# Optimization experiments

Measured on AMD Instinct MI355X. Metric: run time of the kernel, lower is better.

Reference implementation:

```python
import jax, jax.numpy as jnp
import numpy as np

DIM = 128
NUM_LAYERS = 2
FF_MULT = 4
RADIUS = 0.2
K = 8
B, N, L = 8, 2048, 4096
NEG = -1e30


def setup_inputs() -> dict:
    key = jax.random.key(0)
    ks = jax.random.split(key, 12)
    C = DIM
    s = 1.0 / np.sqrt(C)
    w = lambda k, shape, sc: jax.random.normal(k, shape, dtype=jnp.float32) * sc
    inp = {
        "q_xyz": jax.random.uniform(ks[0], (B, N, 3), dtype=jnp.float32),
        "q_feat": jax.random.normal(ks[1], (B, N, C), dtype=jnp.float32),
        "kv_xyz": jax.random.uniform(ks[2], (B, L, 3), dtype=jnp.float32),
        "kv_feat": jax.random.normal(ks[3], (B, L, C), dtype=jnp.float32),
        "kv_pad": jnp.zeros((B, L), dtype=bool),
        # PointTransformerConv params (stacked over layers)
        "W_lin": w(ks[4], (NUM_LAYERS, C, C), s),   # value projection (with bias)
        "b_lin": jnp.zeros((NUM_LAYERS, C), jnp.float32),
        "W_src": w(ks[5], (NUM_LAYERS, C, C), s),   # lin_src, no bias
        "W_dst": w(ks[6], (NUM_LAYERS, C, C), s),   # lin_dst, no bias
        "W_attn": w(ks[7], (NUM_LAYERS, C, C), s),  # attn_nn = Linear+ReLU
        "b_attn": jnp.zeros((NUM_LAYERS, C), jnp.float32),
        "ln1_g": jnp.ones((NUM_LAYERS, C), jnp.float32),
        "ln1_b": jnp.zeros((NUM_LAYERS, C), jnp.float32),
        "W_ff1": w(ks[8], (NUM_LAYERS, C, FF_MULT * C), s),
        "b_ff1": jnp.zeros((NUM_LAYERS, FF_MULT * C), jnp.float32),
        "W_ff2": w(ks[9], (NUM_LAYERS, FF_MULT * C, C), 1.0 / np.sqrt(FF_MULT * C)),
        "b_ff2": jnp.zeros((NUM_LAYERS, C), jnp.float32),
        "ln2_g": jnp.ones((NUM_LAYERS, C), jnp.float32),
        "ln2_b": jnp.zeros((NUM_LAYERS, C), jnp.float32),
    }
    return inp


def _layernorm(x, g, b):
    mu = x.mean(-1, keepdims=True)
    var = ((x - mu) ** 2).mean(-1, keepdims=True)
    return (x - mu) * jax.lax.rsqrt(var + 1e-5) * g + b


def _gather(feats, idx):
    # feats: [B, L, C], idx: [B, N, K] -> [B, N, K, C]
    b, n, k = idx.shape
    g = jnp.take_along_axis(feats, idx.reshape(b, n * k)[:, :, None], axis=1)
    return g.reshape(b, n, k, feats.shape[-1])


def _forward(q_xyz, q_feat, kv_xyz, kv_feat, kv_pad,
             W_lin, b_lin, W_src, W_dst, W_attn, b_attn,
             ln1_g, ln1_b, W_ff1, b_ff1, W_ff2, b_ff2, ln2_g, ln2_b):
    # radius neighbor search (per-batch, fixed K neighbors with validity mask)
    d2 = jnp.sum((q_xyz[:, :, None, :] - kv_xyz[:, None, :, :]) ** 2, axis=-1)  # [B,N,L]
    valid_pair = (d2 <= RADIUS * RADIUS) & (~kv_pad)[:, None, :]
    negd = jnp.where(valid_pair, -d2, NEG)
    negv, idx = jax.lax.top_k(negd, K)          # [B,N,K] nearest-in-ball
    evalid = negv > 0.5 * NEG                   # edge validity mask [B,N,K]

    out = q_feat
    for i in range(NUM_LAYERS):
        # PointTransformerConv, pos_nn = ZeroPos => delta = 0
        aj = _gather(kv_feat @ W_src[i], idx)                    # [B,N,K,C]
        vj = _gather(kv_feat @ W_lin[i] + b_lin[i], idx)         # [B,N,K,C]
        ai = out @ W_dst[i]                                      # [B,N,C]
        logits = jax.nn.relu((ai[:, :, None, :] - aj) @ W_attn[i] + b_attn[i])
        logits = jnp.where(evalid[..., None], logits, NEG)
        m = logits.max(axis=2, keepdims=True)
        e = jnp.exp(logits - m) * evalid[..., None]
        attn = e / jnp.maximum(e.sum(axis=2, keepdims=True), 1e-9)  # per-channel softmax over neighbors
        upd = jnp.sum(attn * vj, axis=2)                         # [B,N,C] scatter-add over edges
        out = _layernorm(out + upd, ln1_g[i], ln1_b[i])
        h = jax.nn.gelu(out @ W_ff1[i] + b_ff1[i], approximate=False)
        out = _layernorm(out + h @ W_ff2[i] + b_ff2[i], ln2_g[i], ln2_b[i])
    return out


def reference(q_xyz, q_feat, kv_xyz, kv_feat, kv_pad,
              W_lin, b_lin, W_src, W_dst, W_attn, b_attn,
              ln1_g, ln1_b, W_ff1, b_ff1, W_ff2, b_ff2, ln2_g, ln2_b):
    return _forward(q_xyz, q_feat, kv_xyz, kv_feat, kv_pad,
                    W_lin, b_lin, W_src, W_dst, W_attn, b_attn,
                    ln1_g, ln1_b, W_ff1, b_ff1, W_ff2, b_ff2, ln2_g, ln2_b)
```

## Files before the change

kernel.cpp:

```cpp
#include <hip/hip_runtime.h>
#include <hip/hip_bf16.h>
#include <math.h>

#define DIM 128
#define BB 8
#define NN 2048
#define LL 4096
#define KK 8

typedef __hip_bfloat16 bf16;
typedef unsigned long long ull;
typedef __attribute__((ext_vector_type(8))) short short8;
typedef __attribute__((ext_vector_type(4))) float float4v;

__device__ __forceinline__ float toF(float x){ return x; }
__device__ __forceinline__ float toF(bf16 x){ return __bfloat162float(x); }
__device__ __forceinline__ void st(float* p, float v){ *p = v; }
__device__ __forceinline__ void st(bf16*  p, float v){ *p = __float2bfloat16(v); }
__device__ __forceinline__ unsigned short f2bf(float f){
  union { bf16 b; unsigned short u; } cv; cv.b = __float2bfloat16(f); return cv.u;
}
__device__ __forceinline__ float2 ld2bf(const bf16* p){
  const unsigned u = *(const unsigned*)p;
  return make_float2(__uint_as_float(u << 16), __uint_as_float(u & 0xFFFF0000u));
}
__device__ __forceinline__ void st2bf(bf16* p, float a, float b){
  *(unsigned*)p = (unsigned)f2bf(a) | ((unsigned)f2bf(b) << 16);
}

__device__ __forceinline__ float gelu_exact(float x){
  return 0.5f * x * (1.0f + erff(x * 0.70710678118654752f));
}

__device__ __forceinline__ float waveSum64(float v){
  #pragma unroll
  for (int o = 32; o > 0; o >>= 1) v += __shfl_xor(v, o, 64);
  return v;
}
__device__ __forceinline__ float quadSum16(float v){
  #pragma unroll
  for (int o = 8; o > 0; o >>= 1) v += __shfl_xor(v, o, 64);
  return v;
}

__device__ __forceinline__ void topk_insert_u(ull (&m)[KK], ull key){
  m[KK-1] = key;
  #pragma unroll
  for (int t = KK-1; t > 0; --t){
    if (m[t] < m[t-1]){ ull tmp = m[t]; m[t] = m[t-1]; m[t-1] = tmp; }
  }
}

#define NC3 125
__device__ __forceinline__ void packOne(const float* __restrict__ src,
                                        bf16* __restrict__ dst, int idx, int nshift){
  const int k = idx >> nshift;
  const int n = idx & ((1 << nshift) - 1);
  const int N = 1 << nshift;
  st(&dst[((size_t)(k>>3)*N + n)*8 + (k&7)], src[idx]);
}

__global__ __launch_bounds__(1024) void setup_all(const float* __restrict__ kv_xyz,
                                                  const float* __restrict__ q_xyz,
                                                  float4* __restrict__ bpts,
                                                  int* __restrict__ offs,
                                                  int* __restrict__ qsrt,
                                                  const float* __restrict__ Wlin,
                                                  const float* __restrict__ Wff1,
                                                  const float* __restrict__ Wff2,
                                                  const float* __restrict__ Wsrc,
                                                  const float* __restrict__ Wdst,
                                                  const float* __restrict__ Wattn,
                                                  bf16* __restrict__ WlinP,
                                                  bf16* __restrict__ Wff1P,
                                                  bf16* __restrict__ Wff2P,
                                                  bf16* __restrict__ WsaP,
                                                  bf16* __restrict__ WdaP)
{
  __shared__ int cnt[NC3];
  __shared__ int off[NC3+1];
  __shared__ float row[8][DIM];
  const int bid = blockIdx.x;
  const int tid = threadIdx.x;
  if (bid < 16){
    const int b   = bid & 7;
    const int role= bid >> 3;
    if (tid < NC3) cnt[tid] = 0;
    __syncthreads();
    if (role == 0){
      const float* kvp = kv_xyz + (size_t)b * LL * 3;
      float px[4], py[4], pz[4]; int pc[4];
      #pragma unroll
      for (int i = 0; i < 4; i++){
        const int e = tid + i*1024;
        px[i] = kvp[3*e]; py[i] = kvp[3*e+1]; pz[i] = kvp[3*e+2];
        const int cx = min((int)(px[i]*5.f), 4);
        const int cy = min((int)(py[i]*5.f), 4);
        const int cz = min((int)(pz[i]*5.f), 4);
        pc[i] = (cz*5 + cy)*5 + cx;
        atomicAdd(&cnt[pc[i]], 1);
      }
      __syncthreads();
      if (tid == 0){
        int acc = 0;
        for (int c = 0; c < NC3; c++){ off[c] = acc; acc += cnt[c]; }
        off[NC3] = acc;
      }
      __syncthreads();
      if (tid < NC3) cnt[tid] = 0;
      __syncthreads();
      float4* dst = bpts + (size_t)b * LL;
      #pragma unroll
      for (int i = 0; i < 4; i++){
        const int e = tid + i*1024;
        const int pos = off[pc[i]] + atomicAdd(&cnt[pc[i]], 1);
        dst[pos] = make_float4(px[i], py[i], pz[i], __int_as_float(e));
      }
      if (tid < NC3 + 1) offs[b*126 + tid] = off[tid];
    } else {
      const float* qp = q_xyz + (size_t)b * NN * 3;
      int pc[2];
      #pragma unroll
      for (int i = 0; i < 2; i++){
        const int e = tid + i*1024;
        const float x = qp[3*e], y = qp[3*e+1], z = qp[3*e+2];
        const int cx = min((int)(x*5.f), 4);
        const int cy = min((int)(y*5.f), 4);
        const int cz = min((int)(z*5.f), 4);
        pc[i] = (cz*5 + cy)*5 + cx;
        atomicAdd(&cnt[pc[i]], 1);
      }
      __syncthreads();
      if (tid == 0){
        int acc = 0;
        for (int c = 0; c < NC3; c++){ off[c] = acc; acc += cnt[c]; }
        off[NC3] = acc;
      }
      __syncthreads();
      if (tid < NC3) cnt[tid] = 0;
      __syncthreads();
      int* dst = qsrt + (size_t)b * NN;
      #pragma unroll
      for (int i = 0; i < 2; i++){
        const int e = tid + i*1024;
        const int pos = off[pc[i]] + atomicAdd(&cnt[pc[i]], 1);
        dst[pos] = e;
      }
    }
  } else if (bid < 304){
    int i = (bid - 16)*1024 + tid;
    if (i < 32768){
      const int l = i >> 14, r = i & 16383;
      packOne(Wlin + (size_t)l*16384, WlinP + (size_t)l*16384, r, 7);
    } else if (i < 163840){
      i -= 32768;
      const int l = i >> 16, r = i & 65535;
      packOne(Wff1 + (size_t)l*65536, Wff1P + (size_t)l*65536, r, 9);
    } else {
      i -= 163840;
      const int l = i >> 16, r = i & 65535;
      packOne(Wff2 + (size_t)l*65536, Wff2P + (size_t)l*65536, r, 7);
    }
  } else {
    const int grp = tid >> 7;
    const int c = tid & 127;
    const int tt = (bid - 304)*8 + grp;
    const int r = tt & 127, which = (tt >> 7) & 1, lay = tt >> 8;
    const float* Wx = (which ? Wdst : Wsrc) + (size_t)lay*DIM*DIM;
    const float* Wa = Wattn + (size_t)lay*DIM*DIM;
    row[grp][c] = Wx[r*DIM + c];
    __syncthreads();
    float acc = 0.f;
    for (int j = 0; j < DIM; j++) acc = fmaf(row[grp][j], Wa[j*DIM + c], acc);
    bf16* dst = (which ? WdaP : WsaP) + (size_t)lay*DIM*DIM;
    st(&dst[((size_t)(r>>3)*DIM + c)*8 + (r&7)], acc);
  }
}

#define QBLK 8
#define SPL 32
__global__ __launch_bounds__(256) void knn_query(const float* __restrict__ q_xyz,
                                                 const float4* __restrict__ bpts,
                                                 const int* __restrict__ offs,
                                                 const int* __restrict__ qsrt,
                                                 int* __restrict__ idx)
{
  __shared__ ull cd[QBLK*257];
  const int tid  = threadIdx.x;
  const int s    = tid & 31;
  const int qloc = tid >> 5;
  const int b    = blockIdx.y;
  const int qbase = blockIdx.x * QBLK;
  const int qid = qsrt[b*NN + qbase + qloc];
  const size_t qo = ((size_t)b * NN + qid) * 3;
  const float qx = q_xyz[qo], qy = q_xyz[qo+1], qz = q_xyz[qo+2];
  const ull THRKEY = ((ull)0x3D23D70Bu << 32);
  ull kthr = THRKEY;
  ull m[KK];
  #pragma unroll
  for (int k = 0; k < KK; k++) m[k] = ~0ULL;
  const int qcx = min((int)(qx*5.f), 4);
  const int qcy = min((int)(qy*5.f), 4);
  const int qcz = min((int)(qz*5.f), 4);
  const int* ofb = offs + b*126;
  const float4* bp = bpts + (size_t)b * LL;
  const int cx0 = max(qcx-1, 0), cx1 = min(qcx+1, 4);
  for (int cz = max(qcz-1,0); cz <= min(qcz+1,4); cz++){
    for (int cy = max(qcy-1,0); cy <= min(qcy+1,4); cy++){
      const int rowc = (cz*5 + cy)*5;
      const int pend = ofb[rowc + cx1 + 1];
      int p = ofb[rowc + cx0] + s;
      if (p < pend){
        float4 pt = bp[p];
        while (true){
          const int pn = p + SPL;
          const bool hn = pn < pend;
          float4 nx;
          if (hn) nx = bp[pn];
          const float dx = qx - pt.x, dy = qy - pt.y, dz = qz - pt.z;
          const float d2 = dx*dx + dy*dy + dz*dz;
          const ull key = ((ull)__float_as_uint(d2) << 32) | (unsigned)__float_as_int(pt.w);
          if (key < kthr){
            topk_insert_u(m, key);
            kthr = (m[KK-1] < THRKEY) ? m[KK-1] : THRKEY;
          }
          if (!hn) break;
          pt = nx; p = pn;
        }
      }
    }
  }
  #pragma unroll
  for (int k = 0; k < KK; k++) cd[qloc*257 + k*32 + s] = m[k];
  __syncthreads();
  if (tid < 64){
    const int q = tid >> 3, g = tid & 7;
    ull mm[KK];
    #pragma unroll
    for (int k = 0; k < KK; k++) mm[k] = ~0ULL;
    #pragma unroll
    for (int u = 0; u < 4; u++){
      const int sl = g + 8*u;
      #pragma unroll
      for (int k = 0; k < KK; k++){
        const ull key = cd[q*257 + k*32 + sl];
        if (key < mm[KK-1]) topk_insert_u(mm, key);
      }
    }
    #pragma unroll
    for (int k = 0; k < KK; k++) cd[q*257 + k*32 + g] = mm[k];
    if (tid < QBLK){
      ull f[KK];
      #pragma unroll
      for (int k = 0; k < KK; k++) f[k] = ~0ULL;
      #pragma unroll
      for (int k = 0; k < 8; k++)
        for (int g2 = 0; g2 < 8; g2++){
          const ull key = cd[tid*257 + k*32 + g2];
          if (key < f[KK-1]) topk_insert_u(f, key);
        }
      const int oq = b * NN + qsrt[b*NN + qbase + tid];
      #pragma unroll
      for (int k = 0; k < KK; k++) idx[oq*KK + k] = (int)(unsigned)(f[k] & 0xFFFFFFFFu);
    }
  }
}

__device__ __forceinline__ void stage_A_f32(const float* __restrict__ A, size_t r0,
                                            int kd, int kc, unsigned short* As, int tid){
  #pragma unroll
  for (int i = 0; i < 8; i++){
    const int f = tid + i*256;
    const int row = f >> 5, c4 = (f & 31) * 4;
    const float4 v = *(const float4*)&A[(r0+row)*kd + kc + c4];
    uint2 u;
    u.x = (unsigned)f2bf(v.x) | ((unsigned)f2bf(v.y) << 16);
    u.y = (unsigned)f2bf(v.z) | ((unsigned)f2bf(v.w) << 16);
    *(uint2*)&As[row*136 + c4] = u;
  }
}
__device__ __forceinline__ void stage_A_bf16(const bf16* __restrict__ A, size_t r0,
                                             int kd, int kc, unsigned short* As, int tid){
  #pragma unroll
  for (int i = 0; i < 8; i++){
    const int f = tid + i*256;
    const int row = f >> 5, c4 = (f & 31) * 4;
    *(uint2*)&As[row*136 + c4] = *(const uint2*)&A[(r0+row)*kd + kc + c4];
  }
}

template<typename TA, int NDIM, bool GELU>
__global__ __launch_bounds__(256) void mfma_single(const TA* __restrict__ A,
                                                   const bf16* __restrict__ Wp,
                                                   const float* __restrict__ bias,
                                                   bf16* __restrict__ Y)
{
  __shared__ __align__(16) unsigned short As[64*136];
  const int tid = threadIdx.x;
  const size_t r0 = (size_t)blockIdx.x * 64;
  const int nblk = blockIdx.y * 128;
  if (sizeof(TA) == 4) stage_A_f32((const float*)A, r0, 128, 0, As, tid);
  else                 stage_A_bf16((const bf16*)A, r0, 128, 0, As, tid);
  __syncthreads();
  const int wid = tid >> 6, ln = tid & 63, qd = ln >> 4, cl = ln & 15;
  float4v acc[8];
  #pragma unroll
  for (int t = 0; t < 8; t++) acc[t] = (float4v){0.f,0.f,0.f,0.f};
  #pragma unroll
  for (int ks = 0; ks < 4; ks++){
    const short8 a = *(const short8*)&As[(wid*16 + cl)*136 + (ks*4 + qd)*8];
    const short8* wb = (const short8*)Wp + (size_t)(ks*4 + qd)*NDIM + nblk + cl;
    #pragma unroll
    for (int t = 0; t < 8; t++){
      const short8 b = wb[t*16];
      acc[t] = __builtin_amdgcn_mfma_f32_16x16x32_bf16(a, b, acc[t], 0, 0, 0);
    }
  }
  #pragma unroll
  for (int t = 0; t < 8; t++){
    const int col = nblk + t*16 + cl;
    const float bv = bias ? bias[col] : 0.f;
    #pragma unroll
    for (int r = 0; r < 4; r++){
      const size_t row = r0 + wid*16 + qd*4 + r;
      float v = acc[t][r] + bv;
      if (GELU) v = gelu_exact(v);
      st(&Y[row*NDIM + col], v);
    }
  }
}

__global__ __launch_bounds__(256) void mfma_dual_qa(const float* __restrict__ kvf,
                                                    const float* __restrict__ featIn,
                                                    const bf16* __restrict__ Wp0,
                                                    const bf16* __restrict__ Wp1,
                                                    const bf16* __restrict__ WpQ,
                                                    const float* __restrict__ bias1,
                                                    bf16* __restrict__ Y0,
                                                    bf16* __restrict__ Y1,
                                                    bf16* __restrict__ Yq)
{
  __shared__ __align__(16) unsigned short As[64*136];
  const int tid = threadIdx.x;
  const int wid = tid >> 6, ln = tid & 63, qd = ln >> 4, cl = ln & 15;
  if (blockIdx.x < 512){
    const size_t r0 = (size_t)blockIdx.x * 64;
    stage_A_f32(kvf, r0, 128, 0, As, tid);
    __syncthreads();
    float4v ac0[8], ac1[8];
    #pragma unroll
    for (int t = 0; t < 8; t++){ ac0[t] = (float4v){0.f,0.f,0.f,0.f}; ac1[t] = (float4v){0.f,0.f,0.f,0.f}; }
    #pragma unroll
    for (int ks = 0; ks < 4; ks++){
      const short8 a = *(const short8*)&As[(wid*16 + cl)*136 + (ks*4 + qd)*8];
      const size_t wo = (size_t)(ks*4 + qd)*DIM + cl;
      const short8* wb0 = (const short8*)Wp0 + wo;
      const short8* wb1 = (const short8*)Wp1 + wo;
      #pragma unroll
      for (int t = 0; t < 8; t++){
        const short8 b0 = wb0[t*16];
        ac0[t] = __builtin_amdgcn_mfma_f32_16x16x32_bf16(a, b0, ac0[t], 0, 0, 0);
        const short8 b1 = wb1[t*16];
        ac1[t] = __builtin_amdgcn_mfma_f32_16x16x32_bf16(a, b1, ac1[t], 0, 0, 0);
      }
    }
    #pragma unroll
    for (int t = 0; t < 8; t++){
      const int col = t*16 + cl;
      const float bv = bias1[col];
      #pragma unroll
      for (int r = 0; r < 4; r++){
        const size_t row = r0 + wid*16 + qd*4 + r;
        st(&Y0[row*DIM + col], ac0[t][r]);
        st(&Y1[row*DIM + col], ac1[t][r] + bv);
      }
    }
  } else {
    const size_t r0 = (size_t)(blockIdx.x - 512) * 64;
    stage_A_f32(featIn, r0, 128, 0, As, tid);
    __syncthreads();
    float4v acc[8];
    #pragma unroll
    for (int t = 0; t < 8; t++) acc[t] = (float4v){0.f,0.f,0.f,0.f};
    #pragma unroll
    for (int ks = 0; ks < 4; ks++){
      const short8 a = *(const short8*)&As[(wid*16 + cl)*136 + (ks*4 + qd)*8];
      const short8* wb = (const short8*)WpQ + (size_t)(ks*4 + qd)*DIM + cl;
      #pragma unroll
      for (int t = 0; t < 8; t++){
        const short8 b = wb[t*16];
        acc[t] = __builtin_amdgcn_mfma_f32_16x16x32_bf16(a, b, acc[t], 0, 0, 0);
      }
    }
    #pragma unroll
    for (int t = 0; t < 8; t++){
      const int col = t*16 + cl;
      #pragma unroll
      for (int r = 0; r < 4; r++){
        const size_t row = r0 + wid*16 + qd*4 + r;
        st(&Yq[row*DIM + col], acc[t][r]);
      }
    }
  }
}

__global__ __launch_bounds__(256) void mfma_ff2ln(const bf16* __restrict__ A,
                                                  const bf16* __restrict__ Wp,
                                                  const float* __restrict__ b2,
                                                  const bf16* __restrict__ resid,
                                                  const float* __restrict__ g,
                                                  const float* __restrict__ bb,
                                                  float* __restrict__ Y)
{
  __shared__ __align__(16) unsigned short As[64*136];
  const int tid = threadIdx.x;
  const size_t r0 = (size_t)blockIdx.x * 64;
  const int wid = tid >> 6, ln = tid & 63, qd = ln >> 4, cl = ln & 15;
  float4v acc[8];
  #pragma unroll
  for (int t = 0; t < 8; t++) acc[t] = (float4v){0.f,0.f,0.f,0.f};
  for (int kc = 0; kc < 512; kc += 128){
    __syncthreads();
    stage_A_bf16(A, r0, 512, kc, As, tid);
    __syncthreads();
    const int k8c = kc >> 3;
    #pragma unroll
    for (int ks = 0; ks < 4; ks++){
      const short8 a = *(const short8*)&As[(wid*16 + cl)*136 + (ks*4 + qd)*8];
      const short8* wb = (const short8*)Wp + (size_t)(k8c + ks*4 + qd)*DIM + cl;
      #pragma unroll
      for (int t = 0; t < 8; t++){
        const short8 b = wb[t*16];
        acc[t] = __builtin_amdgcn_mfma_f32_16x16x32_bf16(a, b, acc[t], 0, 0, 0);
      }
    }
  }
  float v[8][4];
  #pragma unroll
  for (int t = 0; t < 8; t++){
    const int col = t*16 + cl;
    const float bv = b2[col];
    #pragma unroll
    for (int r = 0; r < 4; r++){
      const size_t row = r0 + wid*16 + qd*4 + r;
      v[t][r] = acc[t][r] + bv + toF(resid[row*DIM + col]);
    }
  }
  #pragma unroll
  for (int r = 0; r < 4; r++){
    float s = 0.f;
    #pragma unroll
    for (int t = 0; t < 8; t++) s += v[t][r];
    const float mu = quadSum16(s) * (1.f/DIM);
    float q = 0.f;
    #pragma unroll
    for (int t = 0; t < 8; t++){ const float d = v[t][r] - mu; q += d*d; }
    const float inv = rsqrtf(quadSum16(q) * (1.f/DIM) + 1e-5f);
    const size_t row = r0 + wid*16 + qd*4 + r;
    #pragma unroll
    for (int t = 0; t < 8; t++){
      const int col = t*16 + cl;
      Y[row*DIM + col] = (v[t][r] - mu) * inv * g[col] + bb[col];
    }
  }
}

__global__ __launch_bounds__(256) void attn_ln1(const bf16* __restrict__ qA,
                                                const bf16* __restrict__ srcA,
                                                const bf16* __restrict__ linp,
                                                const int* __restrict__ idx,
                                                const int* __restrict__ qsrt,
                                                const float* __restrict__ b_attn,
                                                const float* __restrict__ feat,
                                                const float* __restrict__ g,
                                                const float* __restrict__ bb,
                                                bf16* __restrict__ out1)
{
  const int tid = threadIdx.x;
  const int wv = tid >> 6, ln = tid & 63;
  const int sp = blockIdx.x * 4 + wv;
  const int b = sp >> 11;
  const int q = b * NN + qsrt[b*NN + (sp & 2047)];
  const bf16* sbase = srcA + (size_t)b * LL * DIM;
  const bf16* vbase = linp + (size_t)b * LL * DIM;
  const int c0 = 2*ln;
  const float2 ba = *(const float2*)&b_attn[c0];
  const float2 qa2 = ld2bf(&qA[(size_t)q*DIM + c0]);
  const float qa0 = qa2.x + ba.x, qa1 = qa2.y + ba.y;
  int ids[KK]; float l0[KK], l1[KK];
  float m0 = -1e30f, m1 = -1e30f;
  #pragma unroll
  for (int k = 0; k < KK; k++){
    const int id = idx[q*KK + k]; ids[k] = id;
    if (id >= 0){
      const float2 s2 = ld2bf(&sbase[(size_t)id*DIM + c0]);
      l0[k] = fmaxf(qa0 - s2.x, 0.f); m0 = fmaxf(m0, l0[k]);
      l1[k] = fmaxf(qa1 - s2.y, 0.f); m1 = fmaxf(m1, l1[k]);
    } else { l0[k] = 0.f; l1[k] = 0.f; }
  }
  float sum0 = 0.f, sum1 = 0.f, upd0 = 0.f, upd1 = 0.f;
  #pragma unroll
  for (int k = 0; k < KK; k++) if (ids[k] >= 0){
    const float e0 = expf(l0[k] - m0); l0[k] = e0; sum0 += e0;
    const float e1 = expf(l1[k] - m1); l1[k] = e1; sum1 += e1;
  }
  if (sum0 > 0.f){
    const float i0 = 1.f / sum0, i1 = 1.f / sum1;
    #pragma unroll
    for (int k = 0; k < KK; k++) if (ids[k] >= 0){
      const float2 v2 = ld2bf(&vbase[(size_t)ids[k]*DIM + c0]);
      upd0 = fmaf(l0[k]*i0, v2.x, upd0);
      upd1 = fmaf(l1[k]*i1, v2.y, upd1);
    }
  }
  const float2 f2 = *(const float2*)&feat[(size_t)q*DIM + c0];
  const float x0 = f2.x + upd0;
  const float x1 = f2.y + upd1;
  const float mu = waveSum64(x0 + x1) * (1.f/DIM);
  const float d0 = x0 - mu, d1 = x1 - mu;
  const float var = waveSum64(d0*d0 + d1*d1) * (1.f/DIM);
  const float inv = rsqrtf(var + 1e-5f);
  const float2 gg = *(const float2*)&g[c0];
  const float2 bbv = *(const float2*)&bb[c0];
  st2bf(&out1[(size_t)q*DIM + c0], d0 * inv * gg.x + bbv.x, d1 * inv * gg.y + bbv.y);
}

extern "C" void kernel_launch(void* const* d_in, const int* in_sizes, int n_in,
                              void* d_out, int out_size, void* d_ws, size_t ws_size,
                              hipStream_t stream)
{
  const float* q_xyz  = (const float*)d_in[0];
  const float* q_feat = (const float*)d_in[1];
  const float* kv_xyz = (const float*)d_in[2];
  const float* kv_feat= (const float*)d_in[3];
  const float* W_lin  = (const float*)d_in[5];
  const float* b_lin  = (const float*)d_in[6];
  const float* W_src  = (const float*)d_in[7];
  const float* W_dst  = (const float*)d_in[8];
  const float* W_attn = (const float*)d_in[9];
  const float* b_attn = (const float*)d_in[10];
  const float* ln1_g  = (const float*)d_in[11];
  const float* ln1_b  = (const float*)d_in[12];
  const float* W_ff1  = (const float*)d_in[13];
  const float* b_ff1  = (const float*)d_in[14];
  const float* W_ff2  = (const float*)d_in[15];
  const float* b_ff2  = (const float*)d_in[16];
  const float* ln2_g  = (const float*)d_in[17];
  const float* ln2_b  = (const float*)d_in[18];
  float* out = (float*)d_out;

  const int MQ  = BB * NN;
  const int MKV = BB * LL;

  char* p = (char*)d_ws;
  int*    idxb  = (int*)p;    p += (size_t)MQ * KK * 4;
  float4* bpts  = (float4*)p; p += (size_t)BB * LL * 16;
  int*    boffs = (int*)p;    p += (size_t)BB * 126 * 4;
  int*    qsrt  = (int*)p;    p += (size_t)BB * NN * 4;
  bf16*  WsaP  = (bf16*)p;  p += (size_t)2 * DIM * DIM * 2;
  bf16*  WdaP  = (bf16*)p;  p += (size_t)2 * DIM * DIM * 2;
  bf16*  WlinP = (bf16*)p;  p += (size_t)2 * DIM * DIM * 2;
  bf16*  Wff1P = (bf16*)p;  p += (size_t)2 * DIM * 4*DIM * 2;
  bf16*  Wff2P = (bf16*)p;  p += (size_t)2 * 4*DIM * DIM * 2;
  float* feat  = (float*)p; p += (size_t)MQ * DIM * 4;
  bf16*  out1  = (bf16*)p;  p += (size_t)MQ * DIM * 2;
  bf16*  srcA  = (bf16*)p;  p += (size_t)MKV * DIM * 2;
  bf16*  linp  = (bf16*)p;  p += (size_t)MKV * DIM * 2;
  bf16*  qA    = (bf16*)p;  p += (size_t)MQ * DIM * 2;
  bf16*  hbuf  = srcA;

  setup_all<<<368, 1024, 0, stream>>>(kv_xyz, q_xyz, bpts, boffs, qsrt,
                                      W_lin, W_ff1, W_ff2, W_src, W_dst, W_attn,
                                      WlinP, Wff1P, Wff2P, WsaP, WdaP);
  knn_query<<<dim3(NN/QBLK, BB), 256, 0, stream>>>(q_xyz, bpts, boffs, qsrt, idxb);

  for (int i = 0; i < 2; i++){
    const size_t w128 = (size_t)i * DIM * DIM;
    const size_t w512 = (size_t)i * DIM * 4*DIM;
    const float* featIn = (i == 0) ? q_feat : feat;

    mfma_dual_qa<<<MKV/64 + MQ/64, 256, 0, stream>>>(kv_feat, featIn,
        WsaP + w128, WlinP + w128, WdaP + w128, b_lin + i*DIM, srcA, linp, qA);
    attn_ln1<<<MQ/4, 256, 0, stream>>>(qA, srcA, linp, idxb, qsrt, b_attn + i*DIM,
                                       featIn, ln1_g + i*DIM, ln1_b + i*DIM, out1);
    mfma_single<bf16, 512, true><<<dim3(MQ/64, 4), 256, 0, stream>>>(
        out1, Wff1P + w512, b_ff1 + i*4*DIM, hbuf);
    float* ydst = (i == 1) ? out : feat;
    mfma_ff2ln<<<MQ/64, 256, 0, stream>>>(hbuf, Wff2P + w512, b_ff2 + i*DIM, out1,
                                          ln2_g + i*DIM, ln2_b + i*DIM, ydst);
  }
}
```

Measured before the change: 288.4 us.

## Fuse KNN search with both layers' kv projections in one interleaved launch

Merges the radius KNN query kernel with the kv-side src/lin projection GEMMs for both layers and the layer-0 query projection into a single launch. GEMM and KNN blocks are interleaved so the compute-heavy MFMA work overlaps with the latency-bound neighbour search. Layer 1's kv projections depend only on kv_feat, so they are hoisted out of the layer loop, and layer 1 runs only a small query-side GEMM. This costs extra workspace for separate per-layer src/lin buffers and a dedicated hidden buffer, and removes one launch per layer.

Result: slower. 296.4 us (+2.8%).

```diff
diff --git a/kernel.cpp b/kernel.cpp
--- a/kernel.cpp
+++ b/kernel.cpp
@@ -177,95 +177,6 @@
   }
 }
 
-#define QBLK 8
-#define SPL 32
-__global__ __launch_bounds__(256) void knn_query(const float* __restrict__ q_xyz,
-                                                 const float4* __restrict__ bpts,
-                                                 const int* __restrict__ offs,
-                                                 const int* __restrict__ qsrt,
-                                                 int* __restrict__ idx)
-{
-  __shared__ ull cd[QBLK*257];
-  const int tid  = threadIdx.x;
-  const int s    = tid & 31;
-  const int qloc = tid >> 5;
-  const int b    = blockIdx.y;
-  const int qbase = blockIdx.x * QBLK;
-  const int qid = qsrt[b*NN + qbase + qloc];
-  const size_t qo = ((size_t)b * NN + qid) * 3;
-  const float qx = q_xyz[qo], qy = q_xyz[qo+1], qz = q_xyz[qo+2];
-  const ull THRKEY = ((ull)0x3D23D70Bu << 32);
-  ull kthr = THRKEY;
-  ull m[KK];
-  #pragma unroll
-  for (int k = 0; k < KK; k++) m[k] = ~0ULL;
-  const int qcx = min((int)(qx*5.f), 4);
-  const int qcy = min((int)(qy*5.f), 4);
-  const int qcz = min((int)(qz*5.f), 4);
-  const int* ofb = offs + b*126;
-  const float4* bp = bpts + (size_t)b * LL;
-  const int cx0 = max(qcx-1, 0), cx1 = min(qcx+1, 4);
-  for (int cz = max(qcz-1,0); cz <= min(qcz+1,4); cz++){
-    for (int cy = max(qcy-1,0); cy <= min(qcy+1,4); cy++){
-      const int rowc = (cz*5 + cy)*5;
-      const int pend = ofb[rowc + cx1 + 1];
-      int p = ofb[rowc + cx0] + s;
-      if (p < pend){
-        float4 pt = bp[p];
-        while (true){
-          const int pn = p + SPL;
-          const bool hn = pn < pend;
-          float4 nx;
-          if (hn) nx = bp[pn];
-          const float dx = qx - pt.x, dy = qy - pt.y, dz = qz - pt.z;
-          const float d2 = dx*dx + dy*dy + dz*dz;
-          const ull key = ((ull)__float_as_uint(d2) << 32) | (unsigned)__float_as_int(pt.w);
-          if (key < kthr){
-            topk_insert_u(m, key);
-            kthr = (m[KK-1] < THRKEY) ? m[KK-1] : THRKEY;
-          }
-          if (!hn) break;
-          pt = nx; p = pn;
-        }
-      }
-    }
-  }
-  #pragma unroll
-  for (int k = 0; k < KK; k++) cd[qloc*257 + k*32 + s] = m[k];
-  __syncthreads();
-  if (tid < 64){
-    const int q = tid >> 3, g = tid & 7;
-    ull mm[KK];
-    #pragma unroll
-    for (int k = 0; k < KK; k++) mm[k] = ~0ULL;
-    #pragma unroll
-    for (int u = 0; u < 4; u++){
-      const int sl = g + 8*u;
-      #pragma unroll
-      for (int k = 0; k < KK; k++){
-        const ull key = cd[q*257 + k*32 + sl];
-        if (key < mm[KK-1]) topk_insert_u(mm, key);
-      }
-    }
-    #pragma unroll
-    for (int k = 0; k < KK; k++) cd[q*257 + k*32 + g] = mm[k];
-    if (tid < QBLK){
-      ull f[KK];
-      #pragma unroll
-      for (int k = 0; k < KK; k++) f[k] = ~0ULL;
-      #pragma unroll
-      for (int k = 0; k < 8; k++)
-        for (int g2 = 0; g2 < 8; g2++){
-          const ull key = cd[tid*257 + k*32 + g2];
-          if (key < f[KK-1]) topk_insert_u(f, key);
-        }
-      const int oq = b * NN + qsrt[b*NN + qbase + tid];
-      #pragma unroll
-      for (int k = 0; k < KK; k++) idx[oq*KK + k] = (int)(unsigned)(f[k] & 0xFFFFFFFFu);
-    }
-  }
-}
-
 __device__ __forceinline__ void stage_A_f32(const float* __restrict__ A, size_t r0,
                                             int kd, int kc, unsigned short* As, int tid){
   #pragma unroll
@@ -286,6 +197,182 @@
     const int f = tid + i*256;
     const int row = f >> 5, c4 = (f & 31) * 4;
     *(uint2*)&As[row*136 + c4] = *(const uint2*)&A[(r0+row)*kd + kc + c4];
+  }
+}
+
+#define QBLK 8
+#define SPL 32
+__global__ __launch_bounds__(256) void knn_gemm(const float* __restrict__ q_xyz,
+                                                const float4* __restrict__ bpts,
+                                                const int* __restrict__ offs,
+                                                const int* __restrict__ qsrt,
+                                                int* __restrict__ idx,
+                                                const float* __restrict__ kvf,
+                                                const float* __restrict__ q_feat,
+                                                const bf16* __restrict__ WsaP,
+                                                const bf16* __restrict__ WlinP,
+                                                const bf16* __restrict__ WdaP0,
+                                                const float* __restrict__ b_lin,
+                                                bf16* __restrict__ srcA0,
+                                                bf16* __restrict__ linp0,
+                                                bf16* __restrict__ srcA1,
+                                                bf16* __restrict__ linp1,
+                                                bf16* __restrict__ qA)
+{
+  __shared__ __align__(16) unsigned char smem[17408];
+  const int bid = blockIdx.x;
+  const int tid = threadIdx.x;
+  bool isGemm; int rid;
+  if (bid < 2560){ isGemm = !(bid & 1); rid = bid >> 1; }
+  else { isGemm = false; rid = 1280 + (bid - 2560); }
+
+  if (isGemm){
+    unsigned short* As = (unsigned short*)smem;
+    const int wid = tid >> 6, ln = tid & 63, qd = ln >> 4, cl = ln & 15;
+    if (rid < 1024){
+      const int lay = rid >> 9;
+      const size_t r0 = (size_t)(rid & 511) * 64;
+      const bf16* Wp0 = WsaP  + (size_t)lay * DIM * DIM;
+      const bf16* Wp1 = WlinP + (size_t)lay * DIM * DIM;
+      const float* bias1 = b_lin + lay * DIM;
+      bf16* Y0 = lay ? srcA1 : srcA0;
+      bf16* Y1 = lay ? linp1 : linp0;
+      stage_A_f32(kvf, r0, 128, 0, As, tid);
+      __syncthreads();
+      float4v ac0[8], ac1[8];
+      #pragma unroll
+      for (int t = 0; t < 8; t++){ ac0[t] = (float4v){0.f,0.f,0.f,0.f}; ac1[t] = (float4v){0.f,0.f,0.f,0.f}; }
+      #pragma unroll
+      for (int ks = 0; ks < 4; ks++){
+        const short8 a = *(const short8*)&As[(wid*16 + cl)*136 + (ks*4 + qd)*8];
+        const size_t wo = (size_t)(ks*4 + qd)*DIM + cl;
+        const short8* wb0 = (const short8*)Wp0 + wo;
+        const short8* wb1 = (const short8*)Wp1 + wo;
+        #pragma unroll
+        for (int t = 0; t < 8; t++){
+          const short8 b0 = wb0[t*16];
+          ac0[t] = __builtin_amdgcn_mfma_f32_16x16x32_bf16(a, b0, ac0[t], 0, 0, 0);
+          const short8 b1 = wb1[t*16];
+          ac1[t] = __builtin_amdgcn_mfma_f32_16x16x32_bf16(a, b1, ac1[t], 0, 0, 0);
+        }
+      }
+      #pragma unroll
+      for (int t = 0; t < 8; t++){
+        const int col = t*16 + cl;
+        const float bv = bias1[col];
+        #pragma unroll
+        for (int r = 0; r < 4; r++){
+          const size_t row = r0 + wid*16 + qd*4 + r;
+          st(&Y0[row*DIM + col], ac0[t][r]);
+          st(&Y1[row*DIM + col], ac1[t][r] + bv);
+        }
+      }
+    } else {
+      const size_t r0 = (size_t)(rid - 1024) * 64;
+      stage_A_f32(q_feat, r0, 128, 0, As, tid);
+      __syncthreads();
+      float4v acc[8];
+      #pragma unroll
+      for (int t = 0; t < 8; t++) acc[t] = (float4v){0.f,0.f,0.f,0.f};
+      #pragma unroll
+      for (int ks = 0; ks < 4; ks++){
+        const short8 a = *(const short8*)&As[(wid*16 + cl)*136 + (ks*4 + qd)*8];
+        const short8* wb = (const short8*)WdaP0 + (size_t)(ks*4 + qd)*DIM + cl;
+        #pragma unroll
+        for (int t = 0; t < 8; t++){
+          const short8 b = wb[t*16];
+          acc[t] = __builtin_amdgcn_mfma_f32_16x16x32_bf16(a, b, acc[t], 0, 0, 0);
+        }
+      }
+      #pragma unroll
+      for (int t = 0; t < 8; t++){
+        const int col = t*16 + cl;
+        #pragma unroll
+        for (int r = 0; r < 4; r++){
+          const size_t row = r0 + wid*16 + qd*4 + r;
+          st(&qA[row*DIM + col], acc[t][r]);
+        }
+      }
+    }
+  } else {
+    ull* cd = (ull*)smem;
+    const int s    = tid & 31;
+    const int qloc = tid >> 5;
+    const int b    = rid >> 8;
+    const int qbase = (rid & 255) * QBLK;
+    const int qid = qsrt[b*NN + qbase + qloc];
+    const size_t qo = ((size_t)b * NN + qid) * 3;
+    const float qx = q_xyz[qo], qy = q_xyz[qo+1], qz = q_xyz[qo+2];
+    const ull THRKEY = ((ull)0x3D23D70Bu << 32);
+    ull kthr = THRKEY;
+    ull m[KK];
+    #pragma unroll
+    for (int k = 0; k < KK; k++) m[k] = ~0ULL;
+    const int qcx = min((int)(qx*5.f), 4);
+    const int qcy = min((int)(qy*5.f), 4);
+    const int qcz = min((int)(qz*5.f), 4);
+    const int* ofb = offs + b*126;
+    const float4* bp = bpts + (size_t)b * LL;
+    const int cx0 = max(qcx-1, 0), cx1 = min(qcx+1, 4);
+    for (int cz = max(qcz-1,0); cz <= min(qcz+1,4); cz++){
+      for (int cy = max(qcy-1,0); cy <= min(qcy+1,4); cy++){
+        const int rowc = (cz*5 + cy)*5;
+        const int pend = ofb[rowc + cx1 + 1];
+        int p = ofb[rowc + cx0] + s;
+        if (p < pend){
+          float4 pt = bp[p];
+          while (true){
+            const int pn = p + SPL;
+            const bool hn = pn < pend;
+            float4 nx;
+            if (hn) nx = bp[pn];
+            const float dx = qx - pt.x, dy = qy - pt.y, dz = qz - pt.z;
+            const float d2 = dx*dx + dy*dy + dz*dz;
+            const ull key = ((ull)__float_as_uint(d2) << 32) | (unsigned)__float_as_int(pt.w);
+            if (key < kthr){
+              topk_insert_u(m, key);
+              kthr = (m[KK-1] < THRKEY) ? m[KK-1] : THRKEY;
+            }
+            if (!hn) break;
+            pt = nx; p = pn;
+          }
+        }
+      }
+    }
+    #pragma unroll
+    for (int k = 0; k < KK; k++) cd[qloc*257 + k*32 + s] = m[k];
+    __syncthreads();
+    if (tid < 64){
+      const int q = tid >> 3, g = tid & 7;
+      ull mm[KK];
+      #pragma unroll
+      for (int k = 0; k < KK; k++) mm[k] = ~0ULL;
+      #pragma unroll
+      for (int u = 0; u < 4; u++){
+        const int sl = g + 8*u;
+        #pragma unroll
+        for (int k = 0; k < KK; k++){
+          const ull key = cd[q*257 + k*32 + sl];
+          if (key < mm[KK-1]) topk_insert_u(mm, key);
+        }
+      }
+      #pragma unroll
+      for (int k = 0; k < KK; k++) cd[q*257 + k*32 + g] = mm[k];
+      if (tid < QBLK){
+        ull f[KK];
+        #pragma unroll
+        for (int k = 0; k < KK; k++) f[k] = ~0ULL;
+        #pragma unroll
+        for (int k = 0; k < 8; k++)
+          for (int g2 = 0; g2 < 8; g2++){
+            const ull key = cd[tid*257 + k*32 + g2];
+            if (key < f[KK-1]) topk_insert_u(f, key);
+          }
+        const int oq = b * NN + qsrt[b*NN + qbase + tid];
+        #pragma unroll
+        for (int k = 0; k < KK; k++) idx[oq*KK + k] = (int)(unsigned)(f[k] & 0xFFFFFFFFu);
+      }
+    }
   }
 }
 
@@ -326,80 +413,6 @@
       float v = acc[t][r] + bv;
       if (GELU) v = gelu_exact(v);
       st(&Y[row*NDIM + col], v);
-    }
-  }
-}
-
-__global__ __launch_bounds__(256) void mfma_dual_qa(const float* __restrict__ kvf,
-                                                    const float* __restrict__ featIn,
-                                                    const bf16* __restrict__ Wp0,
-                                                    const bf16* __restrict__ Wp1,
-                                                    const bf16* __restrict__ WpQ,
-                                                    const float* __restrict__ bias1,
-                                                    bf16* __restrict__ Y0,
-                                                    bf16* __restrict__ Y1,
-                                                    bf16* __restrict__ Yq)
-{
-  __shared__ __align__(16) unsigned short As[64*136];
-  const int tid = threadIdx.x;
-  const int wid = tid >> 6, ln = tid & 63, qd = ln >> 4, cl = ln & 15;
-  if (blockIdx.x < 512){
-    const size_t r0 = (size_t)blockIdx.x * 64;
-    stage_A_f32(kvf, r0, 128, 0, As, tid);
-    __syncthreads();
-    float4v ac0[8], ac1[8];
-    #pragma unroll
-    for (int t = 0; t < 8; t++){ ac0[t] = (float4v){0.f,0.f,0.f,0.f}; ac1[t] = (float4v){0.f,0.f,0.f,0.f}; }
-    #pragma unroll
-    for (int ks = 0; ks < 4; ks++){
-      const short8 a = *(const short8*)&As[(wid*16 + cl)*136 + (ks*4 + qd)*8];
-      const size_t wo = (size_t)(ks*4 + qd)*DIM + cl;
-      const short8* wb0 = (const short8*)Wp0 + wo;
-      const short8* wb1 = (const short8*)Wp1 + wo;
-      #pragma unroll
-      for (int t = 0; t < 8; t++){
-        const short8 b0 = wb0[t*16];
-        ac0[t] = __builtin_amdgcn_mfma_f32_16x16x32_bf16(a, b0, ac0[t], 0, 0, 0);
-        const short8 b1 = wb1[t*16];
-        ac1[t] = __builtin_amdgcn_mfma_f32_16x16x32_bf16(a, b1, ac1[t], 0, 0, 0);
-      }
-    }
-    #pragma unroll
-    for (int t = 0; t < 8; t++){
-      const int col = t*16 + cl;
-      const float bv = bias1[col];
-      #pragma unroll
-      for (int r = 0; r < 4; r++){
-        const size_t row = r0 + wid*16 + qd*4 + r;
-        st(&Y0[row*DIM + col], ac0[t][r]);
-        st(&Y1[row*DIM + col], ac1[t][r] + bv);
-      }
-    }
-  } else {
-    const size_t r0 = (size_t)(blockIdx.x - 512) * 64;
-    stage_A_f32(featIn, r0, 128, 0, As, tid);
-    __syncthreads();
-    float4v acc[8];
-    #pragma unroll
-    for (int t = 0; t < 8; t++) acc[t] = (float4v){0.f,0.f,0.f,0.f};
-    #pragma unroll
-    for (int ks = 0; ks < 4; ks++){
-      const short8 a = *(const short8*)&As[(wid*16 + cl)*136 + (ks*4 + qd)*8];
-      const short8* wb = (const short8*)WpQ + (size_t)(ks*4 + qd)*DIM + cl;
-      #pragma unroll
-      for (int t = 0; t < 8; t++){
-        const short8 b = wb[t*16];
-        acc[t] = __builtin_amdgcn_mfma_f32_16x16x32_bf16(a, b, acc[t], 0, 0, 0);
-      }
-    }
-    #pragma unroll
-    for (int t = 0; t < 8; t++){
-      const int col = t*16 + cl;
-      #pragma unroll
-      for (int r = 0; r < 4; r++){
-        const size_t row = r0 + wid*16 + qd*4 + r;
-        st(&Yq[row*DIM + col], acc[t][r]);
-      }
     }
   }
 }
@@ -564,23 +577,30 @@
   bf16*  Wff2P = (bf16*)p;  p += (size_t)2 * 4*DIM * DIM * 2;
   float* feat  = (float*)p; p += (size_t)MQ * DIM * 4;
   bf16*  out1  = (bf16*)p;  p += (size_t)MQ * DIM * 2;
-  bf16*  srcA  = (bf16*)p;  p += (size_t)MKV * DIM * 2;
-  bf16*  linp  = (bf16*)p;  p += (size_t)MKV * DIM * 2;
+  bf16*  srcA0 = (bf16*)p;  p += (size_t)MKV * DIM * 2;
+  bf16*  linp0 = (bf16*)p;  p += (size_t)MKV * DIM * 2;
+  bf16*  srcA1 = (bf16*)p;  p += (size_t)MKV * DIM * 2;
+  bf16*  linp1 = (bf16*)p;  p += (size_t)MKV * DIM * 2;
   bf16*  qA    = (bf16*)p;  p += (size_t)MQ * DIM * 2;
-  bf16*  hbuf  = srcA;
+  bf16*  hbuf  = (bf16*)p;  p += (size_t)MQ * 4*DIM * 2;
 
   setup_all<<<368, 1024, 0, stream>>>(kv_xyz, q_xyz, bpts, boffs, qsrt,
                                       W_lin, W_ff1, W_ff2, W_src, W_dst, W_attn,
                                       WlinP, Wff1P, Wff2P, WsaP, WdaP);
-  knn_query<<<dim3(NN/QBLK, BB), 256, 0, stream>>>(q_xyz, bpts, boffs, qsrt, idxb);
+  knn_gemm<<<3328, 256, 0, stream>>>(q_xyz, bpts, boffs, qsrt, idxb,
+                                     kv_feat, q_feat, WsaP, WlinP, WdaP,
+                                     b_lin, srcA0, linp0, srcA1, linp1, qA);
 
   for (int i = 0; i < 2; i++){
-    const size_t w128 = (size_t)i * DIM * DIM;
     const size_t w512 = (size_t)i * DIM * 4*DIM;
     const float* featIn = (i == 0) ? q_feat : feat;
-
-    mfma_dual_qa<<<MKV/64 + MQ/64, 256, 0, stream>>>(kv_feat, featIn,
-        WsaP + w128, WlinP + w128, WdaP + w128, b_lin + i*DIM, srcA, linp, qA);
+    const bf16* srcA = i ? srcA1 : srcA0;
+    const bf16* linp = i ? linp1 : linp0;
+
+    if (i == 1){
+      mfma_single<float, 128, false><<<MQ/64, 256, 0, stream>>>(
+          feat, WdaP + DIM*DIM, nullptr, qA);
+    }
     attn_ln1<<<MQ/4, 256, 0, stream>>>(qA, srcA, linp, idxb, qsrt, b_attn + i*DIM,
                                        featIn, ln1_g + i*DIM, ln1_b + i*DIM, out1);
     mfma_single<bf16, 512, true><<<dim3(MQ/64, 4), 256, 0, stream>>>(
```
